# Performance work log

Measured on AMD Instinct MI355X. Metric: run time of the kernel, lower is better.

The kernel has to match this reference:

```python
import jax, jax.numpy as jnp
import numpy as np
from jax import lax

M, N, D = 4096, 4096, 256
SINKHORN_ITERATIONS = 100
SINKHORN_EPSILON = 0.1
DESC_SCALE = 0.05  # keep exp(S/eps) finite for random descriptors


def setup_inputs() -> dict:
    key = jax.random.key(0)
    k1, k2 = jax.random.split(key)
    d_M_q = jax.random.normal(k1, (M, D), dtype=jnp.float32) * DESC_SCALE
    d_N_r = jax.random.normal(k2, (N, D), dtype=jnp.float32) * DESC_SCALE
    z = jnp.float32(0.5)  # SuperGlue bin_score default
    return {"d_M_q": d_M_q, "d_N_r": d_N_r, "z": z}


def reference(d_M_q, d_N_r, z):
    m, n = d_M_q.shape[0], d_N_r.shape[0]
    # score matrix [M, N]
    S = jnp.einsum('md,nd->mn', d_M_q, d_N_r)
    # augment with dustbin row/col filled with z -> [M+1, N+1]
    dtype = d_M_q.dtype
    last_col = jnp.full((m, 1), z, dtype=dtype)
    last_row = jnp.full((1, n + 1), z, dtype=dtype)
    S_aug = jnp.concatenate([jnp.concatenate([S, last_col], axis=1), last_row], axis=0)
    K = jnp.exp(S_aug / SINKHORN_EPSILON)

    def step(K, _):
        K = K / K.sum(axis=1, keepdims=True)  # row normalize
        K = K / K.sum(axis=0, keepdims=True)  # col normalize
        return K, None

    K, _ = lax.scan(step, K, None, length=SINKHORN_ITERATIONS)
    P = K[:m, :n]
    return P, K
```

## Files before the change

kernel.cpp:

```cpp
#include <hip/hip_runtime.h>
#include <hip/hip_bf16.h>


#define MROWS 4096
#define NCOLS 4096
#define DDIM 256
#define MP1 4097
#define INV_EPS 10.0f
#define NBLK 256
#define XSLOT 4160
#define CTR_DW 25728
#define DONE_DW 3216

typedef __attribute__((ext_vector_type(8))) short bf16x8;
typedef __attribute__((ext_vector_type(4))) float f32x4;
typedef __attribute__((ext_vector_type(2))) float f32x2;
typedef __attribute__((ext_vector_type(4))) unsigned short u16x4;

static __device__ __forceinline__ unsigned short f2bf(float f) {
  __hip_bfloat16 h = __float2bfloat16(f);
  union { __hip_bfloat16 h; unsigned short s; } c;
  c.h = h;
  return c.s;
}

static __device__ __forceinline__ void ld_strip_l2(const float* ps, const float* pd,
                                                   float4& xv, float& xd) {
  asm volatile("global_load_dwordx4 %0, %2, off sc0\n\t"
               "global_load_dword %1, %3, off sc0\n\t"
               "s_waitcnt vmcnt(0)"
               : "=v"(xv), "=v"(xd)
               : "v"(ps), "v"(pd)
               : "memory");
}
static __device__ __forceinline__ void st_coherent(float* p, float x) {
  asm volatile("global_store_dword %0, %1, off sc0 sc1" :: "v"(p), "v"(x) : "memory");
}
static __device__ __forceinline__ unsigned ld_flagc(const unsigned* p) {
  unsigned r;
  asm volatile("global_load_dword %0, %1, off sc0 sc1\n\t"
               "s_waitcnt vmcnt(0)"
               : "=v"(r) : "v"(p) : "memory");
  return r;
}
static __device__ __forceinline__ void st_flag(unsigned* p, unsigned x) {
  asm volatile("global_store_dword %0, %1, off sc0 sc1" :: "v"(p), "v"(x) : "memory");
}

template <int MODE>
__global__ __launch_bounds__(256) void mfma_gemm_kernel(
    const float* __restrict__ Q, const float* __restrict__ R,
    unsigned char* __restrict__ A8, unsigned char* __restrict__ T8,
    float* __restrict__ Kf, float* __restrict__ P,
    const float* __restrict__ u, const float* __restrict__ v)
{
  __shared__ unsigned short Qs[128][40];
  __shared__ unsigned short Rs[128][40];

  const int tid = threadIdx.x;
  const int lane = tid & 63;
  const int wid = tid >> 6;
  const int wy = wid >> 1;
  const int wx = wid & 1;
  const int rb = blockIdx.y * 128;
  const int cb = blockIdx.x * 128;
  const int lr = tid >> 3;
  const int lf = (tid & 7) * 4;

  f32x4 acc[4][4];
#pragma unroll
  for (int m = 0; m < 4; ++m)
#pragma unroll
    for (int n = 0; n < 4; ++n)
      acc[m][n] = (f32x4){0.f, 0.f, 0.f, 0.f};

  for (int k0 = 0; k0 < DDIM; k0 += 32) {
    float4 qv[4], rv[4];
#pragma unroll
    for (int i = 0; i < 4; ++i) {
      qv[i] = *reinterpret_cast<const float4*>(&Q[(size_t)(rb + lr + 32 * i) * DDIM + k0 + lf]);
      rv[i] = *reinterpret_cast<const float4*>(&R[(size_t)(cb + lr + 32 * i) * DDIM + k0 + lf]);
    }
    __syncthreads();
#pragma unroll
    for (int i = 0; i < 4; ++i) {
      u16x4 qs = {f2bf(qv[i].x), f2bf(qv[i].y), f2bf(qv[i].z), f2bf(qv[i].w)};
      u16x4 rs = {f2bf(rv[i].x), f2bf(rv[i].y), f2bf(rv[i].z), f2bf(rv[i].w)};
      *reinterpret_cast<u16x4*>(&Qs[lr + 32 * i][lf]) = qs;
      *reinterpret_cast<u16x4*>(&Rs[lr + 32 * i][lf]) = rs;
    }
    __syncthreads();

    const int ko = (lane >> 4) * 8;
    const int fr = lane & 15;
    bf16x8 af[4], bg[4];
#pragma unroll
    for (int m = 0; m < 4; ++m)
      af[m] = *reinterpret_cast<const bf16x8*>(&Qs[wy * 64 + m * 16 + fr][ko]);
#pragma unroll
    for (int n = 0; n < 4; ++n)
      bg[n] = *reinterpret_cast<const bf16x8*>(&Rs[wx * 64 + n * 16 + fr][ko]);
#pragma unroll
    for (int m = 0; m < 4; ++m)
#pragma unroll
      for (int n = 0; n < 4; ++n)
        acc[m][n] = __builtin_amdgcn_mfma_f32_16x16x32_bf16(af[m], bg[n], acc[m][n], 0, 0, 0);
  }

  const int r0 = (lane >> 4) * 4;
  const int fc = lane & 15;
#pragma unroll
  for (int m = 0; m < 4; ++m) {
    const int row0 = rb + wy * 64 + m * 16 + r0;
    float uu[4];
    if (MODE == 1) {
#pragma unroll
      for (int r = 0; r < 4; ++r) uu[r] = u[row0 + r];
    }
#pragma unroll
    for (int n = 0; n < 4; ++n) {
      const int col = cb + wx * 64 + n * 16 + fc;
      if (MODE == 0) {
        float kv[4];
#pragma unroll
        for (int r = 0; r < 4; ++r) kv[r] = __expf(acc[m][n][r] * INV_EPS);
        int packed = __builtin_amdgcn_cvt_pk_fp8_f32(kv[0], kv[1], 0, false);
        packed = __builtin_amdgcn_cvt_pk_fp8_f32(kv[2], kv[3], packed, true);
        *reinterpret_cast<unsigned int*>(&T8[(size_t)col * NCOLS + row0]) = (unsigned int)packed;
#pragma unroll
        for (int r = 0; r < 4; ++r)
          A8[(size_t)(row0 + r) * NCOLS + col] = (unsigned char)(((unsigned int)packed >> (8 * r)) & 0xffu);
      } else {
        const float vc = v[col];
#pragma unroll
        for (int r = 0; r < 4; ++r) {
          const float kv = __expf(acc[m][n][r] * INV_EPS);
          const float val = uu[r] * kv * vc;
          Kf[(size_t)(row0 + r) * MP1 + col] = val;
          P[(size_t)(row0 + r) * NCOLS + col] = val;
        }
      }
    }
  }
}

__global__ void init_sync_kernel(float* __restrict__ xbuf, unsigned* __restrict__ ctr,
                                 unsigned* __restrict__ done8)
{
  const int i = blockIdx.x * 1024 + threadIdx.x;
  if (i < MP1) xbuf[i] = 1.0f;
  if (i < CTR_DW) ctr[i] = 0u;
  if (i < DONE_DW) done8[i] = 0u;
}

__global__ void edgeK_kernel(const float* __restrict__ zp, float* __restrict__ Kf,
                             const float* __restrict__ u, const float* __restrict__ v)
{
  const int i = blockIdx.x * 256 + threadIdx.x;
  if (i >= MP1) return;
  const float E = __expf(zp[0] * INV_EPS);
  Kf[(size_t)i * MP1 + NCOLS] = u[i] * E * v[NCOLS];
  Kf[(size_t)MROWS * MP1 + i] = u[MROWS] * E * v[i];
}

__global__ __launch_bounds__(1024) void sinkhorn_persist_kernel(
    const unsigned char* __restrict__ A8, const unsigned char* __restrict__ T8,
    float* __restrict__ xbuf, const float* __restrict__ zp,
    unsigned* __restrict__ ctr, unsigned* __restrict__ done8)
{
  __shared__ unsigned char lA[16 * 4096];
  __shared__ unsigned char lT[16 * 4096];
  __shared__ float scratch[2][16][17];
  __shared__ float dscr[2][16];

  const int tid = threadIdx.x;
  const int b = blockIdx.x;
  const int lane = tid & 63;
  const int w = tid >> 6;
  const float E = __expf(zp[0] * INV_EPS);
  const int rev4 = ((lane & 1) << 3) | ((lane & 2) << 1) | ((lane & 4) >> 1) | ((lane & 8) >> 3);

  {
    const uint4* gA = reinterpret_cast<const uint4*>(A8 + (size_t)b * 16 * 4096);
    const uint4* gT = reinterpret_cast<const uint4*>(T8 + (size_t)b * 16 * 4096);
    uint4* sA = reinterpret_cast<uint4*>(lA);
    uint4* sT = reinterpret_cast<uint4*>(lT);
#pragma unroll
    for (int i = 0; i < 4; ++i) {
      sA[tid + 1024 * i] = gA[tid + 1024 * i];
      sT[tid + 1024 * i] = gT[tid + 1024 * i];
    }
  }
  __syncthreads();

  const int c0 = (w << 8) + (lane << 2);

  for (int g = 1; g <= 200; ++g) {
    const unsigned char* Kl = (g & 1) ? lA : lT;
    const float* xin = xbuf + (size_t)(g - 1) * XSLOT;
    float* xout = xbuf + (size_t)g * XSLOT;
    const unsigned need = (unsigned)(g - 1);
    const int sb = g & 1;

    if (w == 0) {
      const unsigned* dp = done8 + (size_t)(g - 1) * 16 + (lane & 7);
      unsigned fv = ld_flagc(dp);
      while (!__all((int)(fv >= need))) {
        __builtin_amdgcn_s_sleep(1);
        fv = ld_flagc(dp);
      }
    }
    __syncthreads();

    float4 xv; float xd;
    ld_strip_l2(xin + c0, xin + 4096, xv, xd);

    float acc[16];
#pragma unroll
    for (int r = 0; r < 16; ++r) {
      const unsigned int aw = *reinterpret_cast<const unsigned int*>(Kl + r * 4096 + c0);
      const f32x2 lo = __builtin_amdgcn_cvt_pk_f32_fp8((int)aw, false);
      const f32x2 hi = __builtin_amdgcn_cvt_pk_f32_fp8((int)aw, true);
      acc[r] = lo.x * xv.x + lo.y * xv.y + hi.x * xv.z + hi.y * xv.w;
    }

    float r8[8], r4[4], r2[2], r1;
    {
      const bool f0 = (lane & 1) != 0;
#pragma unroll
      for (int k = 0; k < 8; ++k) {
        const float send = f0 ? acc[k] : acc[k + 8];
        const float keep = f0 ? acc[k + 8] : acc[k];
        r8[k] = keep + __shfl_xor(send, 1, 64);
      }
      const bool f1 = (lane & 2) != 0;
#pragma unroll
      for (int k = 0; k < 4; ++k) {
        const float send = f1 ? r8[k] : r8[k + 4];
        const float keep = f1 ? r8[k + 4] : r8[k];
        r4[k] = keep + __shfl_xor(send, 2, 64);
      }
      const bool f2 = (lane & 4) != 0;
#pragma unroll
      for (int k = 0; k < 2; ++k) {
        const float send = f2 ? r4[k] : r4[k + 2];
        const float keep = f2 ? r4[k + 2] : r4[k];
        r2[k] = keep + __shfl_xor(send, 4, 64);
      }
      const bool f3 = (lane & 8) != 0;
      {
        const float send = f3 ? r2[0] : r2[1];
        const float keep = f3 ? r2[1] : r2[0];
        r1 = keep + __shfl_xor(send, 8, 64);
      }
      r1 += __shfl_xor(r1, 16, 64);
      r1 += __shfl_xor(r1, 32, 64);
    }
    if (lane < 16) scratch[sb][rev4][w] = r1;

    if (b == 0) {
      float sv = xv.x + xv.y + xv.z + xv.w;
      sv += __shfl_xor(sv, 1, 64);  sv += __shfl_xor(sv, 2, 64);
      sv += __shfl_xor(sv, 4, 64);  sv += __shfl_xor(sv, 8, 64);
      sv += __shfl_xor(sv, 16, 64); sv += __shfl_xor(sv, 32, 64);
      if (lane == 0) dscr[sb][w] = sv;
    }
    __syncthreads();

    if (w == 0) {
      const int rr = lane >> 2, wq = (lane & 3) * 4;
      float s = scratch[sb][rr][wq] + scratch[sb][rr][wq + 1]
              + scratch[sb][rr][wq + 2] + scratch[sb][rr][wq + 3];
      s += __shfl_xor(s, 1, 64);
      s += __shfl_xor(s, 2, 64);
      if ((lane & 3) == 0)
        st_coherent(xout + (b << 4) + rr, 1.0f / (s + E * xd));
      if (b == 0) {
        float t = (lane < 16) ? dscr[sb][lane] : 0.f;
        t += __shfl_xor(t, 1, 64);  t += __shfl_xor(t, 2, 64);
        t += __shfl_xor(t, 4, 64);  t += __shfl_xor(t, 8, 64);
        t += __shfl_xor(t, 16, 64); t += __shfl_xor(t, 32, 64);
        if (lane == 0) st_coherent(xout + 4096, 1.0f / (E * (t + xd)));
      }
      asm volatile("s_waitcnt vmcnt(0)" ::: "memory");
      if (lane == 0) {
        unsigned* cp = ctr + (size_t)g * 128 + ((unsigned)(b >> 5) << 4);
        const unsigned ret = __hip_atomic_fetch_add(cp, 1u, __ATOMIC_RELAXED,
                                                    __HIP_MEMORY_SCOPE_AGENT);
        if (ret == 31u)
          st_flag(done8 + (size_t)g * 16 + (b >> 5), (unsigned)g);
      }
    }
  }
}

extern "C" void kernel_launch(void* const* d_in, const int* in_sizes, int n_in,
                              void* d_out, int out_size, void* d_ws, size_t ws_size,
                              hipStream_t stream) {
  const float* Q = (const float*)d_in[0];
  const float* R = (const float*)d_in[1];
  const float* z = (const float*)d_in[2];

  float* P = (float*)d_out;
  float* Kf = P + (size_t)MROWS * NCOLS;

  unsigned char* A8 = (unsigned char*)d_ws;
  unsigned char* T8 = A8 + (size_t)MROWS * NCOLS;
  float* xbuf = (float*)(T8 + (size_t)MROWS * NCOLS);
  unsigned* ctr = (unsigned*)(xbuf + (size_t)201 * XSLOT);
  unsigned* done8 = ctr + CTR_DW;

  const float* u_final = xbuf + (size_t)199 * XSLOT;
  const float* v_final = xbuf + (size_t)200 * XSLOT;

  mfma_gemm_kernel<0><<<dim3(32, 32), 256, 0, stream>>>(Q, R, A8, T8, nullptr, nullptr, nullptr, nullptr);
  init_sync_kernel<<<26, 1024, 0, stream>>>(xbuf, ctr, done8);
  sinkhorn_persist_kernel<<<NBLK, 1024, 0, stream>>>(A8, T8, xbuf, z, ctr, done8);
  mfma_gemm_kernel<1><<<dim3(32, 32), 256, 0, stream>>>(Q, R, nullptr, nullptr, Kf, P, u_final, v_final);
  edgeK_kernel<<<(MP1 + 255) / 256, 256, 0, stream>>>(z, Kf, u_final, v_final);
}
```

Measured before the change: 1.008 ms.

## Replace per-iteration counters with hierarchical monotonic grid barrier and generation flag

```diff
diff --git a/kernel.cpp b/kernel.cpp
--- a/kernel.cpp
+++ b/kernel.cpp
@@ -9,8 +9,7 @@
 #define INV_EPS 10.0f
 #define NBLK 256
 #define XSLOT 4160
-#define CTR_DW 25728
-#define DONE_DW 3216
+#define BAR_DW 160
 
 typedef __attribute__((ext_vector_type(8))) short bf16x8;
 typedef __attribute__((ext_vector_type(4))) float f32x4;
@@ -24,8 +23,13 @@
   return c.s;
 }
 
-static __device__ __forceinline__ void ld_strip_l2(const float* ps, const float* pd,
-                                                   float4& xv, float& xd) {
+static __device__ __forceinline__ void ld_strip(const float* ps, float4& xv) {
+  asm volatile("global_load_dwordx4 %0, %1, off sc0\n\t"
+               "s_waitcnt vmcnt(0)"
+               : "=v"(xv) : "v"(ps) : "memory");
+}
+static __device__ __forceinline__ void ld_strip_dust(const float* ps, const float* pd,
+                                                     float4& xv, float& xd) {
   asm volatile("global_load_dwordx4 %0, %2, off sc0\n\t"
                "global_load_dword %1, %3, off sc0\n\t"
                "s_waitcnt vmcnt(0)"
@@ -42,9 +46,6 @@
                "s_waitcnt vmcnt(0)"
                : "=v"(r) : "v"(p) : "memory");
   return r;
-}
-static __device__ __forceinline__ void st_flag(unsigned* p, unsigned x) {
-  asm volatile("global_store_dword %0, %1, off sc0 sc1" :: "v"(p), "v"(x) : "memory");
 }
 
 template <int MODE>
@@ -144,13 +145,11 @@
   }
 }
 
-__global__ void init_sync_kernel(float* __restrict__ xbuf, unsigned* __restrict__ ctr,
-                                 unsigned* __restrict__ done8)
+__global__ void init_sync_kernel(float* __restrict__ xbuf, unsigned* __restrict__ bar)
 {
   const int i = blockIdx.x * 1024 + threadIdx.x;
   if (i < MP1) xbuf[i] = 1.0f;
-  if (i < CTR_DW) ctr[i] = 0u;
-  if (i < DONE_DW) done8[i] = 0u;
+  if (i < BAR_DW) bar[i] = 0u;
 }
 
 __global__ void edgeK_kernel(const float* __restrict__ zp, float* __restrict__ Kf,
@@ -166,7 +165,7 @@
 __global__ __launch_bounds__(1024) void sinkhorn_persist_kernel(
     const unsigned char* __restrict__ A8, const unsigned char* __restrict__ T8,
     float* __restrict__ xbuf, const float* __restrict__ zp,
-    unsigned* __restrict__ ctr, unsigned* __restrict__ done8)
+    unsigned* __restrict__ bar)
 {
   __shared__ unsigned char lA[16 * 4096];
   __shared__ unsigned char lT[16 * 4096];
@@ -180,6 +179,10 @@
   const float E = __expf(zp[0] * INV_EPS);
   const int rev4 = ((lane & 1) << 3) | ((lane & 2) << 1) | ((lane & 4) >> 1) | ((lane & 8) >> 3);
 
+  unsigned* cg  = bar + ((b & 7) << 4);
+  unsigned* cm  = bar + 128;
+  unsigned* gen = bar + 144;
+
   {
     const uint4* gA = reinterpret_cast<const uint4*>(A8 + (size_t)b * 16 * 4096);
     const uint4* gT = reinterpret_cast<const uint4*>(T8 + (size_t)b * 16 * 4096);
@@ -202,18 +205,18 @@
     const unsigned need = (unsigned)(g - 1);
     const int sb = g & 1;
 
-    if (w == 0) {
-      const unsigned* dp = done8 + (size_t)(g - 1) * 16 + (lane & 7);
-      unsigned fv = ld_flagc(dp);
-      while (!__all((int)(fv >= need))) {
+    if (tid == 0) {
+      unsigned gv = ld_flagc(gen);
+      while (gv < need) {
         __builtin_amdgcn_s_sleep(1);
-        fv = ld_flagc(dp);
+        gv = ld_flagc(gen);
       }
     }
     __syncthreads();
 
-    float4 xv; float xd;
-    ld_strip_l2(xin + c0, xin + 4096, xv, xd);
+    float4 xv; float xd = 0.f;
+    if (w == 0) ld_strip_dust(xin + c0, xin + 4096, xv, xd);
+    else        ld_strip(xin + c0, xv);
 
     float acc[16];
 #pragma unroll
@@ -284,11 +287,15 @@
       }
       asm volatile("s_waitcnt vmcnt(0)" ::: "memory");
       if (lane == 0) {
-        unsigned* cp = ctr + (size_t)g * 128 + ((unsigned)(b >> 5) << 4);
-        const unsigned ret = __hip_atomic_fetch_add(cp, 1u, __ATOMIC_RELAXED,
+        const unsigned a = __hip_atomic_fetch_add(cg, 1u, __ATOMIC_RELAXED,
+                                                  __HIP_MEMORY_SCOPE_AGENT);
+        if (a == 32u * (unsigned)g - 1u) {
+          const unsigned m = __hip_atomic_fetch_add(cm, 1u, __ATOMIC_RELAXED,
                                                     __HIP_MEMORY_SCOPE_AGENT);
-        if (ret == 31u)
-          st_flag(done8 + (size_t)g * 16 + (b >> 5), (unsigned)g);
+          if (m == 8u * (unsigned)g - 1u)
+            __hip_atomic_store(gen, (unsigned)g, __ATOMIC_RELAXED,
+                               __HIP_MEMORY_SCOPE_AGENT);
+        }
       }
     }
   }
@@ -307,15 +314,14 @@
   unsigned char* A8 = (unsigned char*)d_ws;
   unsigned char* T8 = A8 + (size_t)MROWS * NCOLS;
   float* xbuf = (float*)(T8 + (size_t)MROWS * NCOLS);
-  unsigned* ctr = (unsigned*)(xbuf + (size_t)201 * XSLOT);
-  unsigned* done8 = ctr + CTR_DW;
+  unsigned* bar = (unsigned*)(xbuf + (size_t)201 * XSLOT);
 
   const float* u_final = xbuf + (size_t)199 * XSLOT;
   const float* v_final = xbuf + (size_t)200 * XSLOT;
 
   mfma_gemm_kernel<0><<<dim3(32, 32), 256, 0, stream>>>(Q, R, A8, T8, nullptr, nullptr, nullptr, nullptr);
-  init_sync_kernel<<<26, 1024, 0, stream>>>(xbuf, ctr, done8);
-  sinkhorn_persist_kernel<<<NBLK, 1024, 0, stream>>>(A8, T8, xbuf, z, ctr, done8);
+  init_sync_kernel<<<5, 1024, 0, stream>>>(xbuf, bar);
+  sinkhorn_persist_kernel<<<NBLK, 1024, 0, stream>>>(A8, T8, xbuf, z, bar);
   mfma_gemm_kernel<1><<<dim3(32, 32), 256, 0, stream>>>(Q, R, nullptr, nullptr, Kf, P, u_final, v_final);
   edgeK_kernel<<<(MP1 + 255) / 256, 256, 0, stream>>>(z, Kf, u_final, v_final);
 }
```

Result: slower. 1.044 ms (+3.6%).
